# Kernel optimization log

Measured on AMD Instinct MI355X. Metric: run time of the kernel, lower is better.

## Reference

```python
import jax, jax.numpy as jnp
import numpy as np

N = 64
H = 256
B = 32768
OFF = N * (N - 1) // 2  # 2016


def _mlp_params(key, dims, scale_out=0.05):
    ps = []
    for i, (din, dout) in enumerate(zip(dims[:-1], dims[1:])):
        key, k = jax.random.split(key)
        s = 1.0 / np.sqrt(din)
        ps.append((jax.random.normal(k, (dout, din), jnp.float32) * s,
                   jnp.zeros((dout,), jnp.float32)))
    return ps, key


def setup_inputs() -> dict:
    key = jax.random.key(0)
    key, k = jax.random.split(key)
    x = jax.random.normal(k, (B, N), jnp.float32)
    dp, key = _mlp_params(key, [N, H, H, N])
    op, key = _mlp_params(key, [N, H, H, OFF])
    (Wd1, bd1), (Wd2, bd2), (Wdo, bdo) = dp
    (Wo1, bo1), (Wo2, bo2), (Woo, boo) = op
    return {"input": x,
            "Wd1": Wd1, "bd1": bd1, "Wd2": Wd2, "bd2": bd2, "Wdo": Wdo, "bdo": bdo,
            "Wo1": Wo1, "bo1": bo1, "Wo2": Wo2, "bo2": bo2, "Woo": Woo, "boo": boo}


def reference(input, Wd1, bd1, Wd2, bd2, Wdo, bdo, Wo1, bo1, Wo2, bo2, Woo, boo):
    x0 = input  # [B, N]
    # diag branch: tanh MLP -> N diagonal elements per sample
    x = jnp.tanh(input @ Wd1.T + bd1)
    x = jnp.tanh(x @ Wd2.T + bd2)
    x = x @ Wdo.T + bdo  # [B, N]
    # offdiag branch: tanh MLP -> N(N-1)/2 strictly-lower-tri elements
    z = jnp.tanh(input @ Wo1.T + bo1)
    z = jnp.tanh(z @ Wo2.T + bo2)
    z = z @ Woo.T + boo  # [B, OFF]
    n = x.shape[-1]
    b = x0.shape[0]
    rows, cols = np.tril_indices(n, k=-1)  # static index arrays
    diag = np.arange(n)
    L = jnp.zeros((b, n, n), x.dtype)
    L = L.at[:, rows, cols].set(z)
    L = L.at[:, diag, diag].set(x)
    # D[i] = (L L^T) x0[i] computed as L @ (L^T @ x0) to avoid n x n matmul
    y = jnp.einsum('bkj,bk->bj', L, x0)
    D = jnp.einsum('bij,bj->bi', L, y)
    return D
```

## Files before the change

kernel.cpp:

```cpp
#include <hip/hip_runtime.h>
#include <math.h>


#define B_TOT 32768
#define NDIM  64
#define HDIM  256
#define OFFD  2016
#define GRP_UNITS 67584
#define GRP_BYTES 135168

typedef __bf16 bf16x8 __attribute__((ext_vector_type(8)));
typedef float  f32x4  __attribute__((ext_vector_type(4)));

__device__ __forceinline__ float fast_tanh(float x) {
  float e = __expf(2.f * x);
  return 1.f - 2.f * __builtin_amdgcn_rcpf(e + 1.f);
}
__device__ __forceinline__ float lane_bcast(float v, int l) {
  return __uint_as_float(__builtin_amdgcn_readlane(__float_as_uint(v), l));
}
__device__ __forceinline__ float bf_lo(unsigned w) { return __uint_as_float(w << 16); }
__device__ __forceinline__ float bf_hi(unsigned w) { return __uint_as_float(w & 0xffff0000u); }
__device__ __forceinline__ unsigned bfbits(float f) {
  __bf16 h = (__bf16)f;
  return (unsigned)__builtin_bit_cast(unsigned short, h);
}
__device__ __forceinline__ int rs_of(int i) {
  const int a3 = i & 3;
  return ((i * (i - 1)) >> 1) + 6 * (i >> 2) + ((a3 == 2) ? 3 : (a3 == 3) ? 5 : 0);
}

__device__ __forceinline__ void gload_lds16(const void* g, void* l) {
  __builtin_amdgcn_global_load_lds(
      (const __attribute__((address_space(1))) unsigned*)g,
      (__attribute__((address_space(3))) unsigned*)l, 16, 0, 0);
}

#define MFMA(A, B, C) __builtin_amdgcn_mfma_f32_16x16x32_bf16((A), (B), (C), 0, 0, 0)
#define SB0() __builtin_amdgcn_sched_barrier(0)
#define GOFF(g, row) (((((g) & ~7) | (((g) & 7) ^ ((row) & 7)))) << 4)

__device__ __forceinline__ void cast_range(const float* __restrict__ s,
                                           __bf16* __restrict__ d, int n) {
  int i = blockIdx.x * blockDim.x + threadIdx.x;
  const int stride = gridDim.x * blockDim.x;
  for (; i < n; i += stride) d[i] = (__bf16)s[i];
}
__global__ __launch_bounds__(256) void cast_all_kernel(
    const float* s0, __bf16* d0, int n0, const float* s1, __bf16* d1, int n1,
    const float* s2, __bf16* d2, int n2, const float* s3, __bf16* d3, int n3,
    const float* s4, __bf16* d4, int n4, const float* s5, __bf16* d5, int n5,
    __bf16* d6, int n6) {
  cast_range(s0, d0, n0); cast_range(s1, d1, n1); cast_range(s2, d2, n2);
  cast_range(s3, d3, n3); cast_range(s4, d4, n4); cast_range(s5, d5, n5);
  int i = blockIdx.x * blockDim.x + threadIdx.x;
  const int stride = gridDim.x * blockDim.x;
  for (; i < n6; i += stride) d6[i] = (__bf16)0.f;
}

__device__ __forceinline__ bf16x8 cvt8(const float* __restrict__ p) {
  const float4 u = *(const float4*)p;
  const float4 v = *(const float4*)(p + 4);
  bf16x8 r;
  r[0] = (__bf16)u.x; r[1] = (__bf16)u.y; r[2] = (__bf16)u.z; r[3] = (__bf16)u.w;
  r[4] = (__bf16)v.x; r[5] = (__bf16)v.y; r[6] = (__bf16)v.z; r[7] = (__bf16)v.w;
  return r;
}

#define TRK_SMEM (8192 + 32768 + 32768)

__device__ __forceinline__ void stage_chunk2(const char* wreg, char* wb,
                                             int c, int wave) {
  const char* base = wreg + (size_t)c * 16384;
  char* dst = wb + (c & 1) * 16384;
  const int lane = threadIdx.x & 63;
  const int s0 = wave * 64 + lane;
  const int s1 = s0 + 512;
  if (c < 2) {
    const int r0 = s0 >> 3, q0 = (s0 & 7) ^ (r0 & 7);
    gload_lds16(base + r0 * 128 + (q0 << 4), dst + wave * 1024);
    const int r1 = s1 >> 3, q1 = (s1 & 7) ^ (r1 & 7);
    gload_lds16(base + r1 * 128 + (q1 << 4), dst + (wave + 8) * 1024);
  } else {
    const int r0 = s0 >> 5, g0 = s0 & 31;
    const int q0 = (g0 & 24) | ((g0 & 7) ^ (r0 & 7));
    gload_lds16(base + r0 * 512 + (q0 << 4), dst + wave * 1024);
    const int r1 = s1 >> 5, g1 = s1 & 31;
    const int q1 = (g1 & 24) | ((g1 & 7) ^ (r1 & 7));
    gload_lds16(base + r1 * 512 + (q1 << 4), dst + (wave + 8) * 1024);
  }
}

__global__ __launch_bounds__(512, 2) void off_trunk_kernel(
    const float* __restrict__ x, const __bf16* __restrict__ Wreg,
    const float* __restrict__ bo1, const float* __restrict__ bo2,
    __bf16* __restrict__ g2) {
  extern __shared__ char smem[];
  char* xa  = smem;
  char* act = smem + 8192;
  char* wb  = smem + 40960;
  const char* Wc = (const char*)Wreg;

  const int tid = threadIdx.x;
  const int wave = tid >> 6, lane = tid & 63;
  const int lr = lane & 15, lg = lane >> 4;
  const int sb = blockIdx.x * 64;

  float bv1[2], bv2[8];
#pragma unroll
  for (int cc = 0; cc < 2; ++cc) bv1[cc] = bo1[cc * 128 + wave * 16 + lr];
#pragma unroll
  for (int cc = 0; cc < 8; ++cc) bv2[cc] = bo2[cc * 32 + (wave & 1) * 16 + lr];

  {
    const int s = tid >> 3, g = tid & 7;
    const bf16x8 v = cvt8(x + (size_t)(sb + s) * 64 + g * 8);
    *(bf16x8*)(xa + s * 128 + GOFF(g, s)) = v;
  }
  stage_chunk2(Wc, wb, 0, wave);
  __syncthreads();

#pragma unroll
  for (int cc = 0; cc < 2; ++cc) {
    stage_chunk2(Wc, wb, cc + 1, wave);
    const char* wbp = wb + (cc & 1) * 16384;
    const int brow = wave * 16 + lr;
    const bf16x8 b0 = *(const bf16x8*)(wbp + brow * 128 + GOFF(lg, brow));
    const bf16x8 b1 = *(const bf16x8*)(wbp + brow * 128 + GOFF(4 + lg, brow));
    const int ch = cc * 128 + brow;
#pragma unroll
    for (int m = 0; m < 4; ++m) {
      const int arow = m * 16 + lr;
      const bf16x8 a0 = *(const bf16x8*)(xa + arow * 128 + GOFF(lg, arow));
      const bf16x8 a1 = *(const bf16x8*)(xa + arow * 128 + GOFF(4 + lg, arow));
      f32x4 acc = {0.f, 0.f, 0.f, 0.f};
      acc = MFMA(a0, b0, acc);
      acc = MFMA(a1, b1, acc);
#pragma unroll
      for (int r = 0; r < 4; ++r) {
        const int s = m * 16 + lg * 4 + r;
        *(__bf16*)(act + s * 512 + GOFF(ch >> 3, s) + (ch & 7) * 2) =
            (__bf16)fast_tanh(acc[r] + bv1[cc]);
      }
    }
    __syncthreads();
  }

#pragma unroll
  for (int cc = 0; cc < 8; ++cc) {
    const int c = cc + 2;
    if (c + 1 < 10) stage_chunk2(Wc, wb, c + 1, wave);
    const char* wbp = wb + (c & 1) * 16384;
    const int m = wave >> 1, n = wave & 1;
    const int ch = cc * 32 + n * 16 + lr;
    const int brow = n * 16 + lr;
    const int arow = m * 16 + lr;
    f32x4 acc = {0.f, 0.f, 0.f, 0.f};
#pragma unroll
    for (int ks = 0; ks < 8; ++ks) {
      const int g = ks * 4 + lg;
      const bf16x8 a = *(const bf16x8*)(act + arow * 512 + GOFF(g, arow));
      const bf16x8 b = *(const bf16x8*)(wbp + brow * 512 + GOFF(g, brow));
      acc = MFMA(a, b, acc);
    }
#pragma unroll
    for (int r = 0; r < 4; ++r) {
      const int s = m * 16 + lg * 4 + r;
      g2[(size_t)(sb + s) * 256 + ch] = (__bf16)fast_tanh(acc[r] + bv2[cc]);
    }
    if (cc < 7) __syncthreads();
  }
}

__global__ __launch_bounds__(512, 2) void diag_trunk_kernel(
    const float* __restrict__ x, const __bf16* __restrict__ Wreg,
    const float* __restrict__ bd1, const float* __restrict__ bd2,
    const float* __restrict__ bdo, float* __restrict__ xd) {
  extern __shared__ char smem[];
  char* xa  = smem;
  char* act = smem + 8192;
  char* wb  = smem + 40960;
  const char* Wc = (const char*)Wreg;

  const int tid = threadIdx.x;
  const int wave = tid >> 6, lane = tid & 63;
  const int lr = lane & 15, lg = lane >> 4;
  const int sb = blockIdx.x * 64;

  float bv1[2], bv2[8], bv3[2];
#pragma unroll
  for (int cc = 0; cc < 2; ++cc) bv1[cc] = bd1[cc * 128 + wave * 16 + lr];
#pragma unroll
  for (int cc = 0; cc < 8; ++cc) bv2[cc] = bd2[cc * 32 + (wave & 1) * 16 + lr];
#pragma unroll
  for (int cc = 0; cc < 2; ++cc) bv3[cc] = bdo[cc * 32 + (wave & 1) * 16 + lr];

  {
    const int s = tid >> 3, g = tid & 7;
    const bf16x8 v = cvt8(x + (size_t)(sb + s) * 64 + g * 8);
    *(bf16x8*)(xa + s * 128 + GOFF(g, s)) = v;
  }
  stage_chunk2(Wc, wb, 0, wave);
  __syncthreads();

#pragma unroll
  for (int cc = 0; cc < 2; ++cc) {
    stage_chunk2(Wc, wb, cc + 1, wave);
    const char* wbp = wb + (cc & 1) * 16384;
    const int brow = wave * 16 + lr;
    const bf16x8 b0 = *(const bf16x8*)(wbp + brow * 128 + GOFF(lg, brow));
    const bf16x8 b1 = *(const bf16x8*)(wbp + brow * 128 + GOFF(4 + lg, brow));
    const int ch = cc * 128 + brow;
#pragma unroll
    for (int m = 0; m < 4; ++m) {
      const int arow = m * 16 + lr;
      const bf16x8 a0 = *(const bf16x8*)(xa + arow * 128 + GOFF(lg, arow));
      const bf16x8 a1 = *(const bf16x8*)(xa + arow * 128 + GOFF(4 + lg, arow));
      f32x4 acc = {0.f, 0.f, 0.f, 0.f};
      acc = MFMA(a0, b0, acc);
      acc = MFMA(a1, b1, acc);
#pragma unroll
      for (int r = 0; r < 4; ++r) {
        const int s = m * 16 + lg * 4 + r;
        *(__bf16*)(act + s * 512 + GOFF(ch >> 3, s) + (ch & 7) * 2) =
            (__bf16)fast_tanh(acc[r] + bv1[cc]);
      }
    }
    __syncthreads();
  }

  f32x4 h2v[8];
#pragma unroll
  for (int cc = 0; cc < 8; ++cc) {
    const int c = cc + 2;
    if (c + 1 < 11) stage_chunk2(Wc, wb, c + 1, wave);
    const char* wbp = wb + (c & 1) * 16384;
    const int m = wave >> 1, n = wave & 1;
    const int brow = n * 16 + lr;
    const int arow = m * 16 + lr;
    f32x4 acc = {0.f, 0.f, 0.f, 0.f};
#pragma unroll
    for (int ks = 0; ks < 8; ++ks) {
      const int g = ks * 4 + lg;
      const bf16x8 a = *(const bf16x8*)(act + arow * 512 + GOFF(g, arow));
      const bf16x8 b = *(const bf16x8*)(wbp + brow * 512 + GOFF(g, brow));
      acc = MFMA(a, b, acc);
    }
#pragma unroll
    for (int r = 0; r < 4; ++r) h2v[cc][r] = fast_tanh(acc[r] + bv2[cc]);
    __syncthreads();
  }

  {
    const int m = wave >> 1, n = wave & 1;
#pragma unroll
    for (int cc = 0; cc < 8; ++cc) {
      const int ch = cc * 32 + n * 16 + lr;
#pragma unroll
      for (int r = 0; r < 4; ++r) {
        const int s = m * 16 + lg * 4 + r;
        *(__bf16*)(act + s * 512 + GOFF(ch >> 3, s) + (ch & 7) * 2) =
            (__bf16)h2v[cc][r];
      }
    }
  }
  stage_chunk2(Wc, wb, 11, wave);
  __syncthreads();

#pragma unroll
  for (int cc = 0; cc < 2; ++cc) {
    const char* wbp = wb + ((10 + cc) & 1) * 16384;
    const int m = wave >> 1, n = wave & 1;
    const int ch = cc * 32 + n * 16 + lr;
    const int brow = n * 16 + lr;
    const int arow = m * 16 + lr;
    f32x4 acc = {0.f, 0.f, 0.f, 0.f};
#pragma unroll
    for (int ks = 0; ks < 8; ++ks) {
      const int g = ks * 4 + lg;
      const bf16x8 a = *(const bf16x8*)(act + arow * 512 + GOFF(g, arow));
      const bf16x8 b = *(const bf16x8*)(wbp + brow * 512 + GOFF(g, brow));
      acc = MFMA(a, b, acc);
    }
#pragma unroll
    for (int r = 0; r < 4; ++r) {
      const int s = m * 16 + lg * 4 + r;
      xd[(size_t)(sb + s) * 64 + ch] = acc[r] + bv3[cc];
    }
  }
}

#define LIST_OFF 32768
#define LIST_CAP 160
#define GZ_SMEM  (32768 + 1024)

__global__ __launch_bounds__(256, 4) void gemm_z_kernel(
    const __bf16* __restrict__ g2q, const __bf16* __restrict__ Woob,
    const float* __restrict__ boo, __bf16* __restrict__ zq, int bmper) {
  extern __shared__ char gsm[];
  const int tid = threadIdx.x;
  const int wave = tid >> 6, lane = tid & 63;
  const int lr = lane & 15, lg = lane >> 4;
  const int bm = (blockIdx.x & 7) * bmper + (blockIdx.x >> 7);
  const int bn = (blockIdx.x >> 3) & 15;
  const int wr = wave >> 1, wc = wave & 1;
  const int srl = lane >> 3, sch = lane & 7;

  int* lcnt = (int*)(gsm + LIST_OFF);
  unsigned* llist = (unsigned*)(gsm + LIST_OFF + 4);
  const int base = bn * 128;

#define GZSTAGE(KT)                                                             \
  {                                                                             \
    _Pragma("unroll")                                                           \
    for (int j = 0; j < 4; ++j) {                                               \
      const int row = wave * 32 + j * 8 + srl;                                  \
      const int ka = (KT) * 64 + ((sch ^ (row & 7)) << 3);                      \
      gload_lds16(g2q + (size_t)(bm * 128 + row) * 256 + ka,                    \
                  gsm + wave * 4096 + j * 1024);                                \
      gload_lds16(Woob + (size_t)(bn * 128 + row) * 256 + ka,                   \
                  gsm + 16384 + wave * 4096 + j * 1024);                        \
    }                                                                           \
  }

  float bvf[4];
#pragma unroll
  for (int fc = 0; fc < 4; ++fc) {
    const int col = base + wc * 64 + fc * 16 + lr;
    bvf[fc] = (col < OFFD) ? boo[col] : 0.f;
  }

  f32x4 acc[4][4];
#pragma unroll
  for (int i = 0; i < 4; ++i)
#pragma unroll
    for (int j = 0; j < 4; ++j) acc[i][j] = (f32x4){0.f, 0.f, 0.f, 0.f};

  GZSTAGE(0)
  if (tid == 0) *lcnt = 0;
  __syncthreads();

  for (int gi = tid; gi < 528; gi += 256) {
    const int off0 = gi * 4;
    int i = (int)((1.f + sqrtf((float)(8 * off0 + 1))) * 0.5f);
    if (i > 63) i = 63;
    if (i < 1) i = 1;
    while (i > 1 && rs_of(i) > off0) --i;
    while (i < 63 && rs_of(i + 1) <= off0) ++i;
    const int j0 = off0 - rs_of(i);
    int nv = i - j0;
    if (nv > 4) nv = 4;
    const int c0 = ((i * (i - 1)) >> 1) + j0;
    const int last = c0 + nv - 1;
    if (last >= base && c0 <= base + 127) {
      const int idx = atomicAdd(lcnt, 1);
      if (idx < LIST_CAP)
        llist[idx] = ((unsigned)gi << 16) | ((unsigned)i << 9) |
                     ((unsigned)j0 << 3) | (unsigned)nv;
    }
  }

#pragma unroll
  for (int kt = 0; kt < 4; ++kt) {
    if (kt > 0) {
      GZSTAGE(kt)
      __syncthreads();
    }
    const __bf16* Ab = (const __bf16*)gsm;
    const __bf16* Bb = (const __bf16*)(gsm + 16384);
#pragma unroll
    for (int ks = 0; ks < 2; ++ks) {
      bf16x8 af[4], bfr[4];
#pragma unroll
      for (int f = 0; f < 4; ++f) {
        const int ra = wr * 64 + f * 16 + lr;
        af[f] = *(const bf16x8*)((const char*)Ab + ra * 128 + GOFF(ks * 4 + lg, ra));
        const int rb = wc * 64 + f * 16 + lr;
        bfr[f] = *(const bf16x8*)((const char*)Bb + rb * 128 + GOFF(ks * 4 + lg, rb));
      }
#pragma unroll
      for (int fr = 0; fr < 4; ++fr)
#pragma unroll
        for (int fc = 0; fc < 4; ++fc)
          acc[fr][fc] = MFMA(af[fr], bfr[fc], acc[fr][fc]);
    }
    __syncthreads();
  }

  {
    unsigned long long* Tq = (unsigned long long*)gsm;
#pragma unroll
    for (int fr = 0; fr < 4; ++fr) {
      const int rgrp = wr * 16 + fr * 4 + lg;
#pragma unroll
      for (int fc = 0; fc < 4; ++fc) {
        const int ncol = wc * 64 + fc * 16 + lr;
        const unsigned long long v =
            (unsigned long long)bfbits(acc[fr][fc][0] + bvf[fc]) |
            ((unsigned long long)bfbits(acc[fr][fc][1] + bvf[fc]) << 16) |
            ((unsigned long long)bfbits(acc[fr][fc][2] + bvf[fc]) << 32) |
            ((unsigned long long)bfbits(acc[fr][fc][3] + bvf[fc]) << 48);
        Tq[ncol * 32 + (rgrp ^ (ncol & 7))] = v;
      }
    }
  }
  __syncthreads();

  {
    const unsigned* Tw = (const unsigned*)gsm;
    int nl = *lcnt;
    if (nl > LIST_CAP) nl = LIST_CAP;
    const int p = tid >> 2;
    const int grp = bm * 4 + (p >> 4);
    __bf16* zdst = zq + (size_t)grp * GRP_UNITS + (p & 15) * 4224;
    for (int li = (tid & 3); li < nl; li += 4) {
      const unsigned e = llist[li];
      const int gi = e >> 16;
      const int i = (e >> 9) & 63;
      const int j0 = (e >> 3) & 63;
      const int nv = e & 7;
      const int c0 = ((i * (i - 1)) >> 1) + j0;
      const int lc0 = c0 - base;
      unsigned u[4];
#pragma unroll
      for (int d = 0; d < 4; ++d) {
        const int lc = lc0 + d;
        const bool valid = (d < nv) && (lc >= 0) && (lc <= 127);
        u[d] = valid
                   ? Tw[lc * 64 + (((p >> 1) ^ (lc & 7)) << 1) + (p & 1)]
                   : 0u;
      }
      const bool full = (lc0 >= 0) && (lc0 + nv - 1 <= 127);
      if (full) {
        uint4 w;
        w.x = u[0]; w.y = u[1]; w.z = u[2]; w.w = u[3];
        *(uint4*)(zdst + (size_t)gi * 8) = w;
      } else {
        const bool ownpad = (lc0 + nv - 1 >= 0) && (lc0 + nv - 1 <= 127);
#pragma unroll
        for (int d = 0; d < 4; ++d) {
          const int lc = lc0 + d;
          const bool own =
              (d < nv) ? ((lc >= 0) && (lc <= 127)) : ownpad;
          if (own) *(unsigned*)(zdst + (size_t)gi * 8 + d * 2) = u[d];
        }
      }
    }
  }
}

#define APPLY_SMEM (8 * 8448 + 4096)
__global__ __launch_bounds__(512, 2) void apply_kernel(
    const __bf16* __restrict__ zq, const float* __restrict__ xd,
    const float* __restrict__ x0, float* __restrict__ out, int s0base) {
  extern __shared__ char smem[];
  __bf16* ztb = (__bf16*)smem;
  float* ys2 = (float*)(smem + 8 * 8448);

  const int tid = threadIdx.x;
  const int wave = tid >> 6, lane = tid & 63;
  const int blk = blockIdx.x;
  const int sb = s0base + blk * 16;
  const int s0 = wave * 2, s1 = s0 + 1;

  const float x0vA = x0[(size_t)(sb + s0) * 64 + lane];
  const float x0vB = x0[(size_t)(sb + s1) * 64 + lane];
  const float xdA = xd[(size_t)(sb + s0) * 64 + lane];
  const float xdB = xd[(size_t)(sb + s1) * 64 + lane];

  {
    const char* src = (const char*)zq + (size_t)(blk >> 1) * GRP_BYTES +
                      ((blk & 1) * 8 + wave) * 8448;
    char* dst = smem + wave * 8448;
#pragma unroll
    for (int j = 0; j < 8; ++j)
      gload_lds16(src + j * 1024 + lane * 16, dst + j * 1024);
    if (lane < 16) gload_lds16(src + 8192 + lane * 16, dst + 8192);
  }
  asm volatile("s_waitcnt vmcnt(0)" ::: "memory");
  SB0();

  const __bf16* zpair = ztb + wave * 4224;

  float yA = xdA * x0vA, yB = xdB * x0vB;
  int rs = 0;
#pragma unroll
  for (int k = 1; k < 64; ++k) {
    const unsigned w = *(const unsigned*)(zpair + (rs + lane) * 2);
    const float xkA = lane_bcast(x0vA, k);
    const float xkB = lane_bcast(x0vB, k);
    const bool mvalid = lane < k;
    yA += mvalid ? bf_lo(w) * xkA : 0.f;
    yB += mvalid ? bf_hi(w) * xkB : 0.f;
    rs += (k + 3) & ~3;
  }

  float* yp = ys2 + wave * 128;
  *(float2*)(yp + lane * 2) = make_float2(yA, yB);
  asm volatile("s_waitcnt lgkmcnt(0)" ::: "memory");
  SB0();

  float DA = xdA * yA, DB = xdB * yB;
  float dA1 = 0.f, dB1 = 0.f;
  {
    const int r3 = lane & 3;
    const int rsi = ((lane * (lane - 1)) >> 1) + 6 * (lane >> 2) +
                    ((r3 == 2) ? 3 : (r3 == 3) ? 5 : 0);
    const int cmax = (lane + 3) >> 2;
    const __bf16* zrow = zpair + rsi * 2;
#pragma unroll 4
    for (int c = 0; c < cmax; ++c) {
      const uint4 w = *(const uint4*)(zrow + c * 8);
      const float4 u0 = *(const float4*)(yp + c * 8);
      const float4 u1 = *(const float4*)(yp + c * 8 + 4);
      DA += bf_lo(w.x) * u0.x + bf_lo(w.z) * u1.x;
      dA1 += bf_lo(w.y) * u0.z + bf_lo(w.w) * u1.z;
      DB += bf_hi(w.x) * u0.y + bf_hi(w.z) * u1.y;
      dB1 += bf_hi(w.y) * u0.w + bf_hi(w.w) * u1.w;
    }
  }
  out[(size_t)(sb + s0) * 64 + lane] = DA + dA1;
  out[(size_t)(sb + s1) * 64 + lane] = DB + dB1;
}

extern "C" void kernel_launch(void* const* d_in, const int* in_sizes, int n_in,
                              void* d_out, int out_size, void* d_ws, size_t ws_size,
                              hipStream_t stream) {
  const float* x   = (const float*)d_in[0];
  const float* Wd1 = (const float*)d_in[1];
  const float* bd1 = (const float*)d_in[2];
  const float* Wd2 = (const float*)d_in[3];
  const float* bd2 = (const float*)d_in[4];
  const float* Wdo = (const float*)d_in[5];
  const float* bdo = (const float*)d_in[6];
  const float* Wo1 = (const float*)d_in[7];
  const float* bo1 = (const float*)d_in[8];
  const float* Wo2 = (const float*)d_in[9];
  const float* bo2 = (const float*)d_in[10];
  const float* Woo = (const float*)d_in[11];
  const float* boo = (const float*)d_in[12];
  float* out = (float*)d_out;

  char* ws = (char*)d_ws;
  __bf16* Wcat = (__bf16*)(ws + 0);
  __bf16* Woob = (__bf16*)(ws + 360448);
  __bf16* g2   = (__bf16*)(ws + 1409024);
  float*  xdp  = (float*)(ws + 18186240);
  const size_t zoff = 26574848;
  __bf16* zq   = (__bf16*)(ws + zoff);

  const size_t zcap = (ws_size > zoff) ? (ws_size - zoff) : 0;
  int nslices = 4;
  if (zcap >= (size_t)1024 * GRP_BYTES) nslices = 1;
  else if (zcap >= (size_t)512 * GRP_BYTES) nslices = 2;
  const int QSs = B_TOT / nslices;
  const int nbm = QSs / 128;
  const int bmper = nbm >> 3;

  cast_all_kernel<<<512, 256, 0, stream>>>(
      Wo1, Wcat, HDIM * NDIM,
      Wo2, Wcat + 16384, HDIM * HDIM,
      Wd1, Wcat + 81920, HDIM * NDIM,
      Wd2, Wcat + 98304, HDIM * HDIM,
      Wdo, Wcat + 163840, NDIM * HDIM,
      Woo, Woob, OFFD * HDIM,
      Woob + OFFD * HDIM, 32 * HDIM);

  hipFuncSetAttribute((const void*)off_trunk_kernel,
                      hipFuncAttributeMaxDynamicSharedMemorySize, TRK_SMEM);
  hipFuncSetAttribute((const void*)diag_trunk_kernel,
                      hipFuncAttributeMaxDynamicSharedMemorySize, TRK_SMEM);
  off_trunk_kernel<<<B_TOT / 64, 512, TRK_SMEM, stream>>>(
      x, Wcat, bo1, bo2, g2);
  diag_trunk_kernel<<<B_TOT / 64, 512, TRK_SMEM, stream>>>(
      x, Wcat + 81920, bd1, bd2, bdo, xdp);

  hipFuncSetAttribute((const void*)gemm_z_kernel,
                      hipFuncAttributeMaxDynamicSharedMemorySize, GZ_SMEM);
  hipFuncSetAttribute((const void*)apply_kernel,
                      hipFuncAttributeMaxDynamicSharedMemorySize, APPLY_SMEM);
  for (int s = 0; s < nslices; ++s) {
    gemm_z_kernel<<<nbm * 16, 256, GZ_SMEM, stream>>>(
        g2 + (size_t)s * QSs * HDIM, Woob, boo, zq, bmper);
    apply_kernel<<<QSs / 16, 512, APPLY_SMEM, stream>>>(zq, xdp, x, out, s * QSs);
  }
}
```

Before: 154.8 us.

## Store Z as plain row-major bf16 instead of packed interleaved pair layout

The GEMM epilogue now writes Z directly from accumulators as row-major bf16 (2048 columns per sample). This removes the LDS transpose, the per-block triangular index list construction and the scattered packed stores. The apply kernel loads each sample's row separately and uses unpadded triangular offsets, with a masked tail in the second triangular product. The cost is uncoalesced 2-byte global stores in the epilogue, a slightly larger Z buffer, and unaligned 16-byte LDS reads in the second pass.

```diff
diff --git a/kernel.cpp b/kernel.cpp
--- a/kernel.cpp
+++ b/kernel.cpp
@@ -6,8 +6,8 @@
 #define NDIM  64
 #define HDIM  256
 #define OFFD  2016
-#define GRP_UNITS 67584
-#define GRP_BYTES 135168
+#define ZCOLS 2048
+#define ZROWB 4096
 
 typedef __bf16 bf16x8 __attribute__((ext_vector_type(8)));
 typedef float  f32x4  __attribute__((ext_vector_type(4)));
@@ -21,14 +21,6 @@
 }
 __device__ __forceinline__ float bf_lo(unsigned w) { return __uint_as_float(w << 16); }
 __device__ __forceinline__ float bf_hi(unsigned w) { return __uint_as_float(w & 0xffff0000u); }
-__device__ __forceinline__ unsigned bfbits(float f) {
-  __bf16 h = (__bf16)f;
-  return (unsigned)__builtin_bit_cast(unsigned short, h);
-}
-__device__ __forceinline__ int rs_of(int i) {
-  const int a3 = i & 3;
-  return ((i * (i - 1)) >> 1) + 6 * (i >> 2) + ((a3 == 2) ? 3 : (a3 == 3) ? 5 : 0);
-}
 
 __device__ __forceinline__ void gload_lds16(const void* g, void* l) {
   __builtin_amdgcn_global_load_lds(
@@ -290,9 +282,7 @@
   }
 }
 
-#define LIST_OFF 32768
-#define LIST_CAP 160
-#define GZ_SMEM  (32768 + 1024)
+#define GZ_SMEM 32768
 
 __global__ __launch_bounds__(256, 4) void gemm_z_kernel(
     const __bf16* __restrict__ g2q, const __bf16* __restrict__ Woob,
@@ -306,10 +296,6 @@
   const int wr = wave >> 1, wc = wave & 1;
   const int srl = lane >> 3, sch = lane & 7;
 
-  int* lcnt = (int*)(gsm + LIST_OFF);
-  unsigned* llist = (unsigned*)(gsm + LIST_OFF + 4);
-  const int base = bn * 128;
-
 #define GZSTAGE(KT)                                                             \
   {                                                                             \
     _Pragma("unroll")                                                           \
@@ -326,7 +312,7 @@
   float bvf[4];
 #pragma unroll
   for (int fc = 0; fc < 4; ++fc) {
-    const int col = base + wc * 64 + fc * 16 + lr;
+    const int col = bn * 128 + wc * 64 + fc * 16 + lr;
     bvf[fc] = (col < OFFD) ? boo[col] : 0.f;
   }
 
@@ -337,28 +323,7 @@
     for (int j = 0; j < 4; ++j) acc[i][j] = (f32x4){0.f, 0.f, 0.f, 0.f};
 
   GZSTAGE(0)
-  if (tid == 0) *lcnt = 0;
   __syncthreads();
-
-  for (int gi = tid; gi < 528; gi += 256) {
-    const int off0 = gi * 4;
-    int i = (int)((1.f + sqrtf((float)(8 * off0 + 1))) * 0.5f);
-    if (i > 63) i = 63;
-    if (i < 1) i = 1;
-    while (i > 1 && rs_of(i) > off0) --i;
-    while (i < 63 && rs_of(i + 1) <= off0) ++i;
-    const int j0 = off0 - rs_of(i);
-    int nv = i - j0;
-    if (nv > 4) nv = 4;
-    const int c0 = ((i * (i - 1)) >> 1) + j0;
-    const int last = c0 + nv - 1;
-    if (last >= base && c0 <= base + 127) {
-      const int idx = atomicAdd(lcnt, 1);
-      if (idx < LIST_CAP)
-        llist[idx] = ((unsigned)gi << 16) | ((unsigned)i << 9) |
-                     ((unsigned)j0 << 3) | (unsigned)nv;
-    }
-  }
 
 #pragma unroll
   for (int kt = 0; kt < 4; ++kt) {
@@ -366,17 +331,17 @@
       GZSTAGE(kt)
       __syncthreads();
     }
-    const __bf16* Ab = (const __bf16*)gsm;
-    const __bf16* Bb = (const __bf16*)(gsm + 16384);
+    const char* Ab = gsm;
+    const char* Bb = gsm + 16384;
 #pragma unroll
     for (int ks = 0; ks < 2; ++ks) {
       bf16x8 af[4], bfr[4];
 #pragma unroll
       for (int f = 0; f < 4; ++f) {
         const int ra = wr * 64 + f * 16 + lr;
-        af[f] = *(const bf16x8*)((const char*)Ab + ra * 128 + GOFF(ks * 4 + lg, ra));
+        af[f] = *(const bf16x8*)(Ab + ra * 128 + GOFF(ks * 4 + lg, ra));
         const int rb = wc * 64 + f * 16 + lr;
-        bfr[f] = *(const bf16x8*)((const char*)Bb + rb * 128 + GOFF(ks * 4 + lg, rb));
+        bfr[f] = *(const bf16x8*)(Bb + rb * 128 + GOFF(ks * 4 + lg, rb));
       }
 #pragma unroll
       for (int fr = 0; fr < 4; ++fr)
@@ -384,83 +349,33 @@
         for (int fc = 0; fc < 4; ++fc)
           acc[fr][fc] = MFMA(af[fr], bfr[fc], acc[fr][fc]);
     }
-    __syncthreads();
-  }
-
-  {
-    unsigned long long* Tq = (unsigned long long*)gsm;
-#pragma unroll
-    for (int fr = 0; fr < 4; ++fr) {
-      const int rgrp = wr * 16 + fr * 4 + lg;
-#pragma unroll
-      for (int fc = 0; fc < 4; ++fc) {
-        const int ncol = wc * 64 + fc * 16 + lr;
-        const unsigned long long v =
-            (unsigned long long)bfbits(acc[fr][fc][0] + bvf[fc]) |
-            ((unsigned long long)bfbits(acc[fr][fc][1] + bvf[fc]) << 16) |
-            ((unsigned long long)bfbits(acc[fr][fc][2] + bvf[fc]) << 32) |
-            ((unsigned long long)bfbits(acc[fr][fc][3] + bvf[fc]) << 48);
-        Tq[ncol * 32 + (rgrp ^ (ncol & 7))] = v;
-      }
-    }
-  }
-  __syncthreads();
-
-  {
-    const unsigned* Tw = (const unsigned*)gsm;
-    int nl = *lcnt;
-    if (nl > LIST_CAP) nl = LIST_CAP;
-    const int p = tid >> 2;
-    const int grp = bm * 4 + (p >> 4);
-    __bf16* zdst = zq + (size_t)grp * GRP_UNITS + (p & 15) * 4224;
-    for (int li = (tid & 3); li < nl; li += 4) {
-      const unsigned e = llist[li];
-      const int gi = e >> 16;
-      const int i = (e >> 9) & 63;
-      const int j0 = (e >> 3) & 63;
-      const int nv = e & 7;
-      const int c0 = ((i * (i - 1)) >> 1) + j0;
-      const int lc0 = c0 - base;
-      unsigned u[4];
-#pragma unroll
-      for (int d = 0; d < 4; ++d) {
-        const int lc = lc0 + d;
-        const bool valid = (d < nv) && (lc >= 0) && (lc <= 127);
-        u[d] = valid
-                   ? Tw[lc * 64 + (((p >> 1) ^ (lc & 7)) << 1) + (p & 1)]
-                   : 0u;
-      }
-      const bool full = (lc0 >= 0) && (lc0 + nv - 1 <= 127);
-      if (full) {
-        uint4 w;
-        w.x = u[0]; w.y = u[1]; w.z = u[2]; w.w = u[3];
-        *(uint4*)(zdst + (size_t)gi * 8) = w;
-      } else {
-        const bool ownpad = (lc0 + nv - 1 >= 0) && (lc0 + nv - 1 <= 127);
-#pragma unroll
-        for (int d = 0; d < 4; ++d) {
-          const int lc = lc0 + d;
-          const bool own =
-              (d < nv) ? ((lc >= 0) && (lc <= 127)) : ownpad;
-          if (own) *(unsigned*)(zdst + (size_t)gi * 8 + d * 2) = u[d];
-        }
-      }
-    }
-  }
-}
-
-#define APPLY_SMEM (8 * 8448 + 4096)
+    if (kt < 3) __syncthreads();
+  }
+
+#pragma unroll
+  for (int fr = 0; fr < 4; ++fr) {
+    const int row0 = bm * 128 + wr * 64 + fr * 16 + lg * 4;
+#pragma unroll
+    for (int fc = 0; fc < 4; ++fc) {
+      const int col = bn * 128 + wc * 64 + fc * 16 + lr;
+      __bf16* p = zq + (size_t)row0 * ZCOLS + col;
+#pragma unroll
+      for (int r = 0; r < 4; ++r)
+        p[(size_t)r * ZCOLS] = (__bf16)(acc[fr][fc][r] + bvf[fc]);
+    }
+  }
+}
+
+#define APPLY_SMEM (65536 + 4096)
 __global__ __launch_bounds__(512, 2) void apply_kernel(
     const __bf16* __restrict__ zq, const float* __restrict__ xd,
     const float* __restrict__ x0, float* __restrict__ out, int s0base) {
   extern __shared__ char smem[];
-  __bf16* ztb = (__bf16*)smem;
-  float* ys2 = (float*)(smem + 8 * 8448);
+  float* ys2 = (float*)(smem + 65536);
 
   const int tid = threadIdx.x;
   const int wave = tid >> 6, lane = tid & 63;
-  const int blk = blockIdx.x;
-  const int sb = s0base + blk * 16;
+  const int sb = s0base + blockIdx.x * 16;
   const int s0 = wave * 2, s1 = s0 + 1;
 
   const float x0vA = x0[(size_t)(sb + s0) * 64 + lane];
@@ -469,58 +384,81 @@
   const float xdB = xd[(size_t)(sb + s1) * 64 + lane];
 
   {
-    const char* src = (const char*)zq + (size_t)(blk >> 1) * GRP_BYTES +
-                      ((blk & 1) * 8 + wave) * 8448;
-    char* dst = smem + wave * 8448;
-#pragma unroll
-    for (int j = 0; j < 8; ++j)
-      gload_lds16(src + j * 1024 + lane * 16, dst + j * 1024);
-    if (lane < 16) gload_lds16(src + 8192 + lane * 16, dst + 8192);
+    const char* srcA = (const char*)(zq + (size_t)(sb + s0) * ZCOLS);
+    char* dstA = smem + wave * 8192;
+#pragma unroll
+    for (int j = 0; j < 4; ++j) {
+      gload_lds16(srcA + j * 1024 + lane * 16, dstA + j * 1024);
+      gload_lds16(srcA + ZROWB + j * 1024 + lane * 16, dstA + 4096 + j * 1024);
+    }
   }
   asm volatile("s_waitcnt vmcnt(0)" ::: "memory");
   SB0();
 
-  const __bf16* zpair = ztb + wave * 4224;
+  const __bf16* zsA = (const __bf16*)(smem + wave * 8192);
+  const __bf16* zsB = zsA + ZCOLS;
 
   float yA = xdA * x0vA, yB = xdB * x0vB;
   int rs = 0;
 #pragma unroll
   for (int k = 1; k < 64; ++k) {
-    const unsigned w = *(const unsigned*)(zpair + (rs + lane) * 2);
+    const float zA = (float)zsA[rs + lane];
+    const float zB = (float)zsB[rs + lane];
     const float xkA = lane_bcast(x0vA, k);
     const float xkB = lane_bcast(x0vB, k);
-    const bool mvalid = lane < k;
-    yA += mvalid ? bf_lo(w) * xkA : 0.f;
-    yB += mvalid ? bf_hi(w) * xkB : 0.f;
-    rs += (k + 3) & ~3;
-  }
-
-  float* yp = ys2 + wave * 128;
-  *(float2*)(yp + lane * 2) = make_float2(yA, yB);
+    const bool mv = lane < k;
+    yA += mv ? zA * xkA : 0.f;
+    yB += mv ? zB * xkB : 0.f;
+    rs += k;
+  }
+
+  float* ypA = ys2 + wave * 128;
+  float* ypB = ypA + 64;
+  ypA[lane] = yA;
+  ypB[lane] = yB;
   asm volatile("s_waitcnt lgkmcnt(0)" ::: "memory");
   SB0();
 
   float DA = xdA * yA, DB = xdB * yB;
-  float dA1 = 0.f, dB1 = 0.f;
   {
-    const int r3 = lane & 3;
-    const int rsi = ((lane * (lane - 1)) >> 1) + 6 * (lane >> 2) +
-                    ((r3 == 2) ? 3 : (r3 == 3) ? 5 : 0);
-    const int cmax = (lane + 3) >> 2;
-    const __bf16* zrow = zpair + rsi * 2;
-#pragma unroll 4
-    for (int c = 0; c < cmax; ++c) {
-      const uint4 w = *(const uint4*)(zrow + c * 8);
-      const float4 u0 = *(const float4*)(yp + c * 8);
-      const float4 u1 = *(const float4*)(yp + c * 8 + 4);
-      DA += bf_lo(w.x) * u0.x + bf_lo(w.z) * u1.x;
-      dA1 += bf_lo(w.y) * u0.z + bf_lo(w.w) * u1.z;
-      DB += bf_hi(w.x) * u0.y + bf_hi(w.z) * u1.y;
-      dB1 += bf_hi(w.y) * u0.w + bf_hi(w.w) * u1.w;
-    }
-  }
-  out[(size_t)(sb + s0) * 64 + lane] = DA + dA1;
-  out[(size_t)(sb + s1) * 64 + lane] = DB + dB1;
+    const int base = (lane * (lane - 1)) >> 1;
+    const int nf = lane >> 3;
+    const int t = lane & 7;
+    const char* zrA = (const char*)zsA + base * 2;
+    const char* zrB = (const char*)zsB + base * 2;
+    for (int c = 0; c < nf; ++c) {
+      const uint4 wA = *(const uint4*)(zrA + c * 16);
+      const uint4 wB = *(const uint4*)(zrB + c * 16);
+      const float4 u0 = *(const float4*)(ypA + c * 8);
+      const float4 u1 = *(const float4*)(ypA + c * 8 + 4);
+      const float4 v0 = *(const float4*)(ypB + c * 8);
+      const float4 v1 = *(const float4*)(ypB + c * 8 + 4);
+      DA += bf_lo(wA.x) * u0.x + bf_hi(wA.x) * u0.y + bf_lo(wA.y) * u0.z +
+            bf_hi(wA.y) * u0.w + bf_lo(wA.z) * u1.x + bf_hi(wA.z) * u1.y +
+            bf_lo(wA.w) * u1.z + bf_hi(wA.w) * u1.w;
+      DB += bf_lo(wB.x) * v0.x + bf_hi(wB.x) * v0.y + bf_lo(wB.y) * v0.z +
+            bf_hi(wB.y) * v0.w + bf_lo(wB.z) * v1.x + bf_hi(wB.z) * v1.y +
+            bf_lo(wB.w) * v1.z + bf_hi(wB.w) * v1.w;
+    }
+    if (t) {
+      const uint4 wA = *(const uint4*)(zrA + nf * 16);
+      const uint4 wB = *(const uint4*)(zrB + nf * 16);
+      const float4 u0 = *(const float4*)(ypA + nf * 8);
+      const float4 u1 = *(const float4*)(ypA + nf * 8 + 4);
+      const float4 v0 = *(const float4*)(ypB + nf * 8);
+      const float4 v1 = *(const float4*)(ypB + nf * 8 + 4);
+      DA += ((0 < t) ? bf_lo(wA.x) * u0.x : 0.f) + ((1 < t) ? bf_hi(wA.x) * u0.y : 0.f) +
+            ((2 < t) ? bf_lo(wA.y) * u0.z : 0.f) + ((3 < t) ? bf_hi(wA.y) * u0.w : 0.f) +
+            ((4 < t) ? bf_lo(wA.z) * u1.x : 0.f) + ((5 < t) ? bf_hi(wA.z) * u1.y : 0.f) +
+            ((6 < t) ? bf_lo(wA.w) * u1.z : 0.f);
+      DB += ((0 < t) ? bf_lo(wB.x) * v0.x : 0.f) + ((1 < t) ? bf_hi(wB.x) * v0.y : 0.f) +
+            ((2 < t) ? bf_lo(wB.y) * v0.z : 0.f) + ((3 < t) ? bf_hi(wB.y) * v0.w : 0.f) +
+            ((4 < t) ? bf_lo(wB.z) * v1.x : 0.f) + ((5 < t) ? bf_hi(wB.z) * v1.y : 0.f) +
+            ((6 < t) ? bf_lo(wB.w) * v1.z : 0.f);
+    }
+  }
+  out[(size_t)(sb + s0) * 64 + lane] = DA;
+  out[(size_t)(sb + s1) * 64 + lane] = DB;
 }
 
 extern "C" void kernel_launch(void* const* d_in, const int* in_sizes, int n_in,
@@ -551,8 +489,8 @@
 
   const size_t zcap = (ws_size > zoff) ? (ws_size - zoff) : 0;
   int nslices = 4;
-  if (zcap >= (size_t)1024 * GRP_BYTES) nslices = 1;
-  else if (zcap >= (size_t)512 * GRP_BYTES) nslices = 2;
+  if (zcap >= (size_t)B_TOT * ZROWB) nslices = 1;
+  else if (zcap >= (size_t)(B_TOT / 2) * ZROWB) nslices = 2;
   const int QSs = B_TOT / nslices;
   const int nbm = QSs / 128;
   const int bmper = nbm >> 3;
```

Result: no change. 152.6 us (-1.4%).
